# Optimization experiments

Hardware: AMD Instinct MI355X
Metric: run time of the kernel (lower is better)

The kernel has to match this reference:

```python
import jax, jax.numpy as jnp
import numpy as np

NUM_HEADS = 8
NUM_LEVELS = 4
NUM_POINTS = 8
EMBED = 256
SPATIAL_SHAPES = ((92, 160), (46, 80), (23, 40), (12, 20))


def _bilinear_sample(vl, gx, gy, H, W):
    # vl: [N, d, H*W]; gx, gy: [N, Q, P], grid coords in [-1, 1]
    # matches F.grid_sample(mode='bilinear', padding_mode='zeros', align_corners=False)
    x = (gx + 1.0) * (W * 0.5) - 0.5
    y = (gy + 1.0) * (H * 0.5) - 0.5
    x0 = jnp.floor(x)
    y0 = jnp.floor(y)
    wx = x - x0
    wy = y - y0
    x0i = x0.astype(jnp.int32)
    y0i = y0.astype(jnp.int32)
    N, Q, P = gx.shape
    d = vl.shape[1]

    def gather(xi, yi):
        valid = ((xi >= 0) & (xi < W) & (yi >= 0) & (yi < H)).astype(vl.dtype)
        idx = jnp.clip(yi, 0, H - 1) * W + jnp.clip(xi, 0, W - 1)  # [N, Q, P]
        flat = jnp.broadcast_to(idx.reshape(N, 1, Q * P), (N, d, Q * P))
        got = jnp.take_along_axis(vl, flat, axis=2).reshape(N, d, Q, P)
        return got * valid[:, None]

    return (gather(x0i, y0i) * ((1 - wx) * (1 - wy))[:, None]
            + gather(x0i + 1, y0i) * (wx * (1 - wy))[:, None]
            + gather(x0i, y0i + 1) * ((1 - wx) * wy)[:, None]
            + gather(x0i + 1, y0i + 1) * (wx * wy)[:, None])


def _forward(query, value, reference_points, spatial_shapes,
             W_off, b_off, W_attn, b_attn, W_val, b_val, W_out, b_out):
    shapes = np.asarray(spatial_shapes)  # static per-level (H, W)
    bs, Q, C = query.shape
    H, Lv, P = NUM_HEADS, NUM_LEVELS, NUM_POINTS
    d = C // H
    # value projection, split into heads: [bs*H, d, Ltot]
    v = value @ W_val + b_val
    v = v.reshape(bs, -1, H, d).transpose(0, 2, 3, 1).reshape(bs * H, d, -1)
    # sampling offsets [bs, Q, H, Lv, P, 2]
    off = (query @ W_off + b_off).reshape(bs, Q, H, Lv, P, 2)
    # attention weights, softmax over Lv*P
    aw = jax.nn.softmax((query @ W_attn + b_attn).reshape(bs, Q, H, Lv * P), axis=-1)
    aw = aw.reshape(bs, Q, H, Lv, P).transpose(0, 2, 1, 3, 4).reshape(bs * H, Q, Lv, P)
    # normalize offsets by level (W, H)
    norm = jnp.asarray([[w_, h_] for h_, w_ in shapes], dtype=query.dtype)  # [Lv, 2]
    loc = reference_points[:, :, None, :, None, :] + off / norm[None, None, None, :, None, :]
    grids = (2.0 * loc - 1.0).transpose(0, 2, 1, 3, 4, 5).reshape(bs * H, Q, Lv, P, 2)
    out = jnp.zeros((bs * H, d, Q), dtype=query.dtype)
    start = 0
    for lvl in range(Lv):
        H_l, W_l = int(shapes[lvl, 0]), int(shapes[lvl, 1])
        vl = v[:, :, start:start + H_l * W_l]
        g = grids[:, :, lvl]  # [bs*H, Q, P, 2]
        s = _bilinear_sample(vl, g[..., 0], g[..., 1], H_l, W_l)  # [bs*H, d, Q, P]
        out = out + jnp.einsum('ndqp,nqp->ndq', s, aw[:, :, lvl])
        start += H_l * W_l
    out = out.reshape(bs, H, d, Q).transpose(0, 3, 1, 2).reshape(bs, Q, C)
    return out @ W_out + b_out


def setup_inputs() -> dict:
    key = jax.random.key(0)
    ks = jax.random.split(key, 9)
    bs, Q = 6, 4096  # 6 cameras x (64x64 BEV queries)
    Ltot = sum(h * w for h, w in SPATIAL_SHAPES)  # 19560
    HLP2 = NUM_HEADS * NUM_LEVELS * NUM_POINTS * 2  # 512
    HLP = NUM_HEADS * NUM_LEVELS * NUM_POINTS  # 256
    s = 0.02
    return {
        "query": jax.random.normal(ks[0], (bs, Q, EMBED), jnp.float32),
        "value": jax.random.normal(ks[1], (bs, Ltot, EMBED), jnp.float32),
        "reference_points": jax.random.uniform(ks[2], (bs, Q, NUM_LEVELS, 2), jnp.float32),
        "spatial_shapes": jnp.asarray(SPATIAL_SHAPES, jnp.int32),
        "W_off": s * jax.random.normal(ks[3], (EMBED, HLP2), jnp.float32),
        "b_off": s * jax.random.normal(ks[4], (HLP2,), jnp.float32),
        "W_attn": s * jax.random.normal(ks[5], (EMBED, HLP), jnp.float32),
        "b_attn": s * jax.random.normal(ks[6], (HLP,), jnp.float32),
        "W_val": s * jax.random.normal(ks[7], (EMBED, EMBED), jnp.float32),
        "b_val": jnp.zeros((EMBED,), jnp.float32),
        "W_out": s * jax.random.normal(ks[8], (EMBED, EMBED), jnp.float32),
        "b_out": jnp.zeros((EMBED,), jnp.float32),
    }


def reference(query, value, reference_points, spatial_shapes,
              W_off, b_off, W_attn, b_attn, W_val, b_val, W_out, b_out):
    return _forward(query, value, reference_points, spatial_shapes,
                    W_off, b_off, W_attn, b_attn, W_val, b_val, W_out, b_out)
```

## Files before the change

kernel.cpp:

```cpp
#include <hip/hip_runtime.h>
#include <hip/hip_fp16.h>
#include <stdint.h>

#define BS 6
#define NQ 4096
#define NH 8
#define EMB 256
#define LTOT 19560
#define ROWS_V 117360
#define ROWS_VP 117376
#define ROWS_Q 24576
#define VB2 1834
#define QB 1152

typedef __attribute__((ext_vector_type(8))) short bf16x8;
typedef __attribute__((ext_vector_type(4))) float floatx4;
typedef __attribute__((ext_vector_type(8))) unsigned short ushort8v;

__device__ __forceinline__ ushort f2bf(float f) {
    union { float f; uint32_t i; } c; c.f = f;
    uint32_t r = c.i + 0x7FFFu + ((c.i >> 16) & 1u);
    return (ushort)(r >> 16);
}
__device__ __forceinline__ ushort f2h(float f) {
    __half h = __float2half(f);
    union { __half h; ushort u; } c; c.h = h; return c.u;
}
__device__ __forceinline__ float h2f(ushort u) {
    union { ushort u; __half h; } c; c.u = u; return __half2float(c.h);
}
__device__ __forceinline__ uint32_t cvtpk(float a, float b) {
    uint32_t r;
    asm("v_cvt_pk_bf16_f32 %0, %1, %2" : "=v"(r) : "v"(a), "v"(b));
    return r;
}

__device__ __forceinline__ void gll16(const ushort* g, ushort* l) {
    __builtin_amdgcn_global_load_lds(
        (const __attribute__((address_space(1))) void*)g,
        (__attribute__((address_space(3))) void*)l, 16, 0, 0);
}

template<int L>
__device__ __forceinline__ float bcastf(float x) {
    return __int_as_float(
        __builtin_amdgcn_ds_swizzle(__float_as_int(x), 0x1C | (L << 5)));
}
template<int L>
__device__ __forceinline__ uint32_t bcastu(uint32_t x) {
    return (uint32_t)__builtin_amdgcn_ds_swizzle((int)x, 0x1C | (L << 5));
}

__device__ __forceinline__ void fmx_lo(float& acc, float w, uint32_t u) {
    asm("v_fma_mix_f32 %0, %1, %2, %0 op_sel:[0,0,0] op_sel_hi:[0,1,0]"
        : "+v"(acc) : "v"(w), "v"(u));
}
__device__ __forceinline__ void fmx_hi(float& acc, float w, uint32_t u) {
    asm("v_fma_mix_f32 %0, %1, %2, %0 op_sel:[0,1,0] op_sel_hi:[0,1,0]"
        : "+v"(acc) : "v"(w), "v"(u));
}

__global__ __launch_bounds__(256) void prep(
    const float* __restrict__ W_val, const float* __restrict__ W_off,
    const float* __restrict__ W_attn, const float* __restrict__ W_out,
    const float* __restrict__ b_off, const float* __restrict__ b_attn,
    ushort* __restrict__ Wvt, ushort* __restrict__ Wq,
    ushort* __restrict__ Wot, float* __restrict__ bcat)
{
    int id = blockIdx.x * 256 + threadIdx.x;
    if (id < 65536) {
        int n = id >> 8, k = id & 255;
        Wvt[id ^ ((n & 7) << 3)] = f2bf(W_val[k * 256 + n]);
        return;
    }
    id -= 65536;
    if (id < 131072) {
        int n = id >> 8, k = id & 255;
        Wq[id ^ ((n & 7) << 3)] = f2bf(W_off[k * 512 + n]);
        return;
    }
    id -= 131072;
    if (id < 65536) {
        int n = id >> 8, k = id & 255;
        Wq[131072 + (id ^ ((n & 7) << 3))] = f2bf(W_attn[k * 256 + n]);
        return;
    }
    id -= 65536;
    if (id < 65536) {
        int n = id >> 8, k = id & 255;
        Wot[id] = f2bf(W_out[k * 256 + n]);
        return;
    }
    id -= 65536;
    if (id < 768) bcat[id] = (id < 512) ? b_off[id] : b_attn[id - 512];
}

__global__ __launch_bounds__(512, 4) void front(
    const float* __restrict__ value,
    const float* __restrict__ query,
    const ushort* __restrict__ Wvt,
    const ushort* __restrict__ Wq,
    const float* __restrict__ b_val,
    const float* __restrict__ bcat,
    ushort* __restrict__ v_out,
    ushort* __restrict__ qp_out)
{
    __shared__ ushort Bs[128 * 256];

    const int t = threadIdx.x;
    const int w = t >> 6;
    const int lane = t & 63;
    const int bid = blockIdx.x;

    const float* Ap;
    const ushort* Bsrc;
    const float* bias;
    ushort* Cout;
    int Nout, bm, bn, Mrows;
    if (bid < VB2) {
        int m = bid >> 1, nh = bid & 1;
        bm = m * 128; bn = nh * 128;
        Ap = value; Bsrc = Wvt + bn * 256; bias = b_val; Cout = v_out;
        Nout = 256; Mrows = ROWS_V;
    } else {
        int qb = bid - VB2;
        int m = qb / 6, nh = qb - m * 6;
        bm = m * 128; bn = nh * 128;
        Ap = query; Bsrc = Wq + bn * 256; bias = bcat; Cout = qp_out;
        Nout = 768; Mrows = ROWS_Q;
    }

    #pragma unroll
    for (int i = 0; i < 8; ++i)
        gll16(Bsrc + i * 4096 + t * 8, &Bs[i * 4096 + t * 8]);
    __syncthreads();

    const int wm = (w >> 2) * 64;
    const int wn = (w & 3) * 32;
    const int ks = (lane >> 4) * 8;
    const int arow0 = bm + wm + (lane & 15);

    const int nl0 = wn + (lane & 15);
    const int bsw = (nl0 & 7) << 3;
    int bbase[2];
    #pragma unroll
    for (int j = 0; j < 2; ++j)
        bbase[j] = (nl0 + j * 16) * 256 + ks;

    const float* arow_p[4];
    bool rok[4];
    #pragma unroll
    for (int i = 0; i < 4; ++i) {
        int r = arow0 + i * 16;
        rok[i] = r < Mrows;
        arow_p[i] = Ap + (size_t)r * 256 + ks;
    }

    floatx4 acc[4][2] = {};

    for (int kt = 0; kt < 256; kt += 32) {
        bf16x8 a[4], b[2];
        #pragma unroll
        for (int i = 0; i < 4; ++i) {
            float4 f0, f1;
            if (rok[i]) {
                f0 = *(const float4*)(arow_p[i] + kt);
                f1 = *(const float4*)(arow_p[i] + kt + 4);
            } else {
                f0 = make_float4(0.f, 0.f, 0.f, 0.f); f1 = f0;
            }
            union { uint32_t u[4]; bf16x8 v; } cc;
            cc.u[0] = cvtpk(f0.x, f0.y);
            cc.u[1] = cvtpk(f0.z, f0.w);
            cc.u[2] = cvtpk(f1.x, f1.y);
            cc.u[3] = cvtpk(f1.z, f1.w);
            a[i] = cc.v;
        }
        #pragma unroll
        for (int j = 0; j < 2; ++j)
            b[j] = *(const bf16x8*)&Bs[(bbase[j] + kt) ^ bsw];
        #pragma unroll
        for (int i = 0; i < 4; ++i)
            #pragma unroll
            for (int j = 0; j < 2; ++j)
                acc[i][j] = __builtin_amdgcn_mfma_f32_16x16x32_bf16(
                    a[i], b[j], acc[i][j], 0, 0, 0);
    }

    const int crow = (lane >> 4) * 4;
    const int ccol = lane & 15;
    #pragma unroll
    for (int j = 0; j < 2; ++j) {
        int gcol = bn + wn + j * 16 + ccol;
        float bv = bias[gcol];
        #pragma unroll
        for (int i = 0; i < 4; ++i) {
            #pragma unroll
            for (int r = 0; r < 4; ++r) {
                int grow = bm + wm + i * 16 + crow + r;
                if (grow < Mrows)
                    Cout[(size_t)grow * Nout + gcol] = f2h(acc[i][j][r] + bv);
            }
        }
    }
}

__global__ __launch_bounds__(256) void gemm_bt(
    const ushort* __restrict__ A,
    const ushort* __restrict__ Bt,
    const float* __restrict__ bias,
    float* __restrict__ C, int M, int N)
{
    constexpr int K = 256;
    __shared__ ushort As[128 * 32];
    __shared__ ushort Bs[128 * 32];

    const int t = threadIdx.x;
    const int w = t >> 6;
    const int lane = t & 63;
    const int bm = blockIdx.x * 128;
    const int bn = blockIdx.y * 128;
    const int wm = (w >> 1) * 64;
    const int wn = (w & 1) * 64;

    floatx4 acc[4][4] = {};

    const int srow = lane >> 2;
    const int scol = (lane & 3) * 8;
    const ushort* Ag0 = A + (size_t)(bm + (w * 2 + 0) * 16 + srow) * K + scol;
    const ushort* Ag1 = A + (size_t)(bm + (w * 2 + 1) * 16 + srow) * K + scol;
    const ushort* Bg0 = Bt + (size_t)(bn + (w * 2 + 0) * 16 + srow) * K + scol;
    const ushort* Bg1 = Bt + (size_t)(bn + (w * 2 + 1) * 16 + srow) * K + scol;
    ushort* Al0 = &As[(w * 2 + 0) * 512];
    ushort* Al1 = &As[(w * 2 + 1) * 512];
    ushort* Bl0 = &Bs[(w * 2 + 0) * 512];
    ushort* Bl1 = &Bs[(w * 2 + 1) * 512];

    const ushort* apt = &As[(wm + (lane & 15)) * 32 + (lane >> 4) * 8];
    const ushort* bpt = &Bs[(wn + (lane & 15)) * 32 + (lane >> 4) * 8];

    for (int kt = 0; kt < K; kt += 32) {
        __syncthreads();
        gll16(Ag0 + kt, Al0);
        gll16(Ag1 + kt, Al1);
        gll16(Bg0 + kt, Bl0);
        gll16(Bg1 + kt, Bl1);
        __syncthreads();

        bf16x8 a[4], b[4];
        #pragma unroll
        for (int i = 0; i < 4; ++i) {
            a[i] = *(const bf16x8*)(apt + i * 16 * 32);
            b[i] = *(const bf16x8*)(bpt + i * 16 * 32);
        }
        #pragma unroll
        for (int i = 0; i < 4; ++i)
            #pragma unroll
            for (int j = 0; j < 4; ++j)
                acc[i][j] = __builtin_amdgcn_mfma_f32_16x16x32_bf16(
                    a[i], b[j], acc[i][j], 0, 0, 0);
    }

    const int crow = (lane >> 4) * 4;
    const int ccol = lane & 15;
    #pragma unroll
    for (int j = 0; j < 4; ++j) {
        int gcol = bn + wn + j * 16 + ccol;
        float bv = bias[gcol];
        #pragma unroll
        for (int i = 0; i < 4; ++i) {
            #pragma unroll
            for (int r = 0; r < 4; ++r) {
                int grow = bm + wm + i * 16 + crow + r;
                if (grow < M)
                    C[(size_t)grow * N + gcol] = acc[i][j][r] + bv;
            }
        }
    }
}

__global__ __launch_bounds__(256) void sampler4(
    const ushort* __restrict__ v,
    const ushort* __restrict__ qp,
    const float* __restrict__ ref,
    ushort* __restrict__ agg)
{
    __shared__ char ballast[49152];
    if (blockIdx.x > 0x7FFFFFF0u) {
        ballast[threadIdx.x] = (char)threadIdx.x;
        agg[0] = (ushort)ballast[(threadIdx.x * 37) & 4095];
    }

    const int bid = (blockIdx.x & 7) * 384 + (blockIdx.x >> 3);

    const int tid = threadIdx.x;
    const int g = bid * 64 + (tid >> 2);
    const int st = tid & 3;
    const int h = g & 7;
    const int bq = g >> 3;
    const int b = bid >> 9;

    const int Wl = 160 >> st;
    const int Hl = (st == 3) ? 12 : (92 >> st);
    const int Sl = (st == 0) ? 0 : (st == 1) ? 14720 : (st == 2) ? 18400 : 19320;

    const ushort* qrow = qp + (size_t)bq * 768;

    float px[8], py[8];
    {
        ushort8v uo0 = *(const ushort8v*)(qrow + h * 64 + st * 16);
        ushort8v uo1 = *(const ushort8v*)(qrow + h * 64 + st * 16 + 8);
        float2 rf = *(const float2*)(ref + (size_t)bq * 8 + st * 2);
        const float fW = (float)Wl, fH = (float)Hl;
        #pragma unroll
        for (int i = 0; i < 4; ++i) {
            px[i]     = fmaf(rf.x, fW, h2f(uo0[2 * i]))     - 0.5f;
            py[i]     = fmaf(rf.y, fH, h2f(uo0[2 * i + 1])) - 0.5f;
            px[i + 4] = fmaf(rf.x, fW, h2f(uo1[2 * i]))     - 0.5f;
            py[i + 4] = fmaf(rf.y, fH, h2f(uo1[2 * i + 1])) - 0.5f;
        }
    }

    float a8[8];
    {
        ushort8v ul = *(const ushort8v*)(qrow + 512 + h * 32 + st * 8);
        #pragma unroll
        for (int i = 0; i < 8; ++i) a8[i] = h2f(ul[i]);
        float m = a8[0];
        #pragma unroll
        for (int i = 1; i < 8; ++i) m = fmaxf(m, a8[i]);
        m = fmaxf(m, __shfl_xor(m, 1, 4));
        m = fmaxf(m, __shfl_xor(m, 2, 4));
        float s = 0.f;
        #pragma unroll
        for (int i = 0; i < 8; ++i) { a8[i] = __expf(a8[i] - m); s += a8[i]; }
        s += __shfl_xor(s, 1, 4);
        s += __shfl_xor(s, 2, 4);
        float inv = 1.f / s;
        #pragma unroll
        for (int i = 0; i < 8; ++i) a8[i] *= inv;
    }

    const char* vb = (const char*)(v + (size_t)b * (LTOT * EMB));
    const uint32_t coffB = (uint32_t)(h * 64 + st * 16);

    float acc[8] = {0.f, 0.f, 0.f, 0.f, 0.f, 0.f, 0.f, 0.f};

    #pragma unroll
    for (int idx = 0; idx < 8; ++idx) {
        float px_ = px[idx], py_ = py[idx];
        float x0f = floorf(px_), y0f = floorf(py_);
        float wx = px_ - x0f, wy = py_ - y0f;
        int x0 = (int)x0f, y0 = (int)y0f;
        int x1 = x0 + 1, y1 = y0 + 1;
        float vx0 = ((uint32_t)x0 < (uint32_t)Wl) ? 1.f : 0.f;
        float vx1 = ((uint32_t)x1 < (uint32_t)Wl) ? 1.f : 0.f;
        float vy0 = ((uint32_t)y0 < (uint32_t)Hl) ? 1.f : 0.f;
        float vy1 = ((uint32_t)y1 < (uint32_t)Hl) ? 1.f : 0.f;
        int cx0 = min(max(x0, 0), Wl - 1);
        int cx1 = min(max(x1, 0), Wl - 1);
        int cy0 = min(max(y0, 0), Hl - 1);
        int cy1 = min(max(y1, 0), Hl - 1);
        float aw = a8[idx];
        float omx = 1.f - wx, omy = 1.f - wy;
        float omya = omy * aw, wya = wy * aw;
        float w00 = omx * omya * (vx0 * vy0);
        float w10 = wx  * omya * (vx1 * vy0);
        float w01 = omx * wya  * (vx0 * vy1);
        float w11 = wx  * wya  * (vx1 * vy1);
        int r0 = Sl + cy0 * Wl;
        int r1 = Sl + cy1 * Wl;
        uint32_t e00 = (uint32_t)(r0 + cx0) << 9;
        uint32_t e10 = (uint32_t)(r0 + cx1) << 9;
        uint32_t e01 = (uint32_t)(r1 + cx0) << 9;
        uint32_t e11 = (uint32_t)(r1 + cx1) << 9;

        #define ACCMIX(w_, c_) \
            fmx_lo(acc[0], w_, c_.x); fmx_hi(acc[1], w_, c_.x); \
            fmx_lo(acc[2], w_, c_.y); fmx_hi(acc[3], w_, c_.y); \
            fmx_lo(acc[4], w_, c_.z); fmx_hi(acc[5], w_, c_.z); \
            fmx_lo(acc[6], w_, c_.w); fmx_hi(acc[7], w_, c_.w);
        #define DO_LEVEL(L) { \
            float W00 = bcastf<L>(w00), W10 = bcastf<L>(w10); \
            float W01 = bcastf<L>(w01), W11 = bcastf<L>(w11); \
            uint32_t E00 = bcastu<L>(e00), E10 = bcastu<L>(e10); \
            uint32_t E01 = bcastu<L>(e01), E11 = bcastu<L>(e11); \
            uint4 c00 = *(const uint4*)(vb + (E00 + coffB)); \
            uint4 c10 = *(const uint4*)(vb + (E10 + coffB)); \
            uint4 c01 = *(const uint4*)(vb + (E01 + coffB)); \
            uint4 c11 = *(const uint4*)(vb + (E11 + coffB)); \
            ACCMIX(W00, c00); ACCMIX(W10, c10); \
            ACCMIX(W01, c01); ACCMIX(W11, c11); }
        DO_LEVEL(0)
        DO_LEVEL(1)
        DO_LEVEL(2)
        DO_LEVEL(3)
        #undef DO_LEVEL
        #undef ACCMIX
    }

    ushort8v r;
    #pragma unroll
    for (int i = 0; i < 8; ++i) r[i] = f2bf(acc[i]);
    *(ushort8v*)(agg + (size_t)bq * 256 + h * 32 + st * 8) = r;
}

extern "C" void kernel_launch(void* const* d_in, const int* in_sizes, int n_in,
                              void* d_out, int out_size, void* d_ws, size_t ws_size,
                              hipStream_t stream) {
    const float* query  = (const float*)d_in[0];
    const float* value  = (const float*)d_in[1];
    const float* refpts = (const float*)d_in[2];
    const float* W_off  = (const float*)d_in[4];
    const float* b_off  = (const float*)d_in[5];
    const float* W_attn = (const float*)d_in[6];
    const float* b_attn = (const float*)d_in[7];
    const float* W_val  = (const float*)d_in[8];
    const float* b_val  = (const float*)d_in[9];
    const float* W_out  = (const float*)d_in[10];
    const float* b_out  = (const float*)d_in[11];
    float* out = (float*)d_out;

    char* ws = (char*)d_ws;
    ushort* v_bf   = (ushort*)(ws);
    ushort* qp     = (ushort*)(ws + 72679424ull);
    ushort* agg_bf = (ushort*)(ws + 148176896ull);
    ushort* Wvt    = (ushort*)(ws + 160759808ull);
    ushort* Wq     = (ushort*)(ws + 160890880ull);
    ushort* Wot    = (ushort*)(ws + 161284096ull);
    float*  bcat   = (float*) (ws + 161415168ull);

    prep<<<1283, 256, 0, stream>>>(W_val, W_off, W_attn, W_out,
                                   b_off, b_attn, Wvt, Wq, Wot, bcat);

    front<<<VB2 + QB, 512, 0, stream>>>(
        value, query, Wvt, Wq, b_val, bcat, v_bf, qp);

    sampler4<<<(ROWS_Q * NH) / 64, 256, 0, stream>>>(
        v_bf, qp, refpts, agg_bf);

    gemm_bt<<<dim3(ROWS_Q / 128, 2), 256, 0, stream>>>(
        agg_bf, Wot, b_out, out, ROWS_Q, 256);
}
```

Measured before the change: 495.7 us.

## Restructure front GEMM to stage activations in LDS, stream weights from global

The front projection kernel used to stage a 128x256 slice of bf16 weights in LDS and have every wave read and convert fp32 activations straight from global memory. Each block now owns 64 rows covering 256 output columns. The block converts those activation rows to bf16 once into swizzled LDS, in two K halves so the second half's conversion overlaps the first half's MFMAs, and each wave reads its weight fragments directly from global/L2. The aim is to stop redundant global reads and bf16 conversions of activation rows across column tiles, at the cost of more global weight traffic and a 256-thread block with a larger accumulator tile.

```diff
diff --git a/kernel.cpp b/kernel.cpp
--- a/kernel.cpp
+++ b/kernel.cpp
@@ -10,8 +10,8 @@
 #define ROWS_V 117360
 #define ROWS_VP 117376
 #define ROWS_Q 24576
-#define VB2 1834
-#define QB 1152
+#define VB 1834
+#define QB3 1152
 
 typedef __attribute__((ext_vector_type(8))) short bf16x8;
 typedef __attribute__((ext_vector_type(4))) float floatx4;
@@ -70,19 +70,19 @@
     int id = blockIdx.x * 256 + threadIdx.x;
     if (id < 65536) {
         int n = id >> 8, k = id & 255;
-        Wvt[id ^ ((n & 7) << 3)] = f2bf(W_val[k * 256 + n]);
+        Wvt[id] = f2bf(W_val[k * 256 + n]);
         return;
     }
     id -= 65536;
     if (id < 131072) {
         int n = id >> 8, k = id & 255;
-        Wq[id ^ ((n & 7) << 3)] = f2bf(W_off[k * 512 + n]);
+        Wq[id] = f2bf(W_off[k * 512 + n]);
         return;
     }
     id -= 131072;
     if (id < 65536) {
         int n = id >> 8, k = id & 255;
-        Wq[131072 + (id ^ ((n & 7) << 3))] = f2bf(W_attn[k * 256 + n]);
+        Wq[131072 + id] = f2bf(W_attn[k * 256 + n]);
         return;
     }
     id -= 65536;
@@ -95,7 +95,7 @@
     if (id < 768) bcat[id] = (id < 512) ? b_off[id] : b_attn[id - 512];
 }
 
-__global__ __launch_bounds__(512, 4) void front(
+__global__ __launch_bounds__(256, 3) void front(
     const float* __restrict__ value,
     const float* __restrict__ query,
     const ushort* __restrict__ Wvt,
@@ -105,99 +105,135 @@
     ushort* __restrict__ v_out,
     ushort* __restrict__ qp_out)
 {
-    __shared__ ushort Bs[128 * 256];
+    __shared__ ushort As[64 * 256];
 
     const int t = threadIdx.x;
     const int w = t >> 6;
     const int lane = t & 63;
     const int bid = blockIdx.x;
 
-    const float* Ap;
-    const ushort* Bsrc;
-    const float* bias;
-    ushort* Cout;
-    int Nout, bm, bn, Mrows;
-    if (bid < VB2) {
-        int m = bid >> 1, nh = bid & 1;
-        bm = m * 128; bn = nh * 128;
-        Ap = value; Bsrc = Wvt + bn * 256; bias = b_val; Cout = v_out;
+    const float* Ap; const ushort* Bt; const float* bias;
+    ushort* Cout; int Nout, bm, bn, Mrows;
+    if (bid < VB) {
+        bm = bid * 64; bn = 0;
+        Ap = value; Bt = Wvt; bias = b_val; Cout = v_out;
         Nout = 256; Mrows = ROWS_V;
     } else {
-        int qb = bid - VB2;
-        int m = qb / 6, nh = qb - m * 6;
-        bm = m * 128; bn = nh * 128;
-        Ap = query; Bsrc = Wq + bn * 256; bias = bcat; Cout = qp_out;
+        int qb = bid - VB;
+        int m = qb / 3, nh = qb - m * 3;
+        bm = m * 64; bn = nh * 256;
+        Ap = query; Bt = Wq + (size_t)bn * 256; bias = bcat; Cout = qp_out;
         Nout = 768; Mrows = ROWS_Q;
     }
 
-    #pragma unroll
-    for (int i = 0; i < 8; ++i)
-        gll16(Bsrc + i * 4096 + t * 8, &Bs[i * 4096 + t * 8]);
+    const int rt = t >> 2;
+    const int jc = t & 3;
+    const bool rv = (bm + rt) < Mrows;
+    const float* Arow = Ap + (size_t)(bm + rt) * 256;
+    ushort* Aw = As + rt * 256;
+    const int rx = (rt & 7) << 3;
+
+    float4 fa[8], fb[8];
+    #pragma unroll
+    for (int i = 0; i < 4; ++i) {
+        int c = jc + i * 4;
+        if (rv) {
+            fa[2 * i]     = *(const float4*)(Arow + c * 8);
+            fa[2 * i + 1] = *(const float4*)(Arow + c * 8 + 4);
+        } else { fa[2 * i] = make_float4(0.f, 0.f, 0.f, 0.f); fa[2 * i + 1] = fa[2 * i]; }
+    }
+    #pragma unroll
+    for (int i = 0; i < 4; ++i) {
+        int c = 16 + jc + i * 4;
+        if (rv) {
+            fb[2 * i]     = *(const float4*)(Arow + c * 8);
+            fb[2 * i + 1] = *(const float4*)(Arow + c * 8 + 4);
+        } else { fb[2 * i] = make_float4(0.f, 0.f, 0.f, 0.f); fb[2 * i + 1] = fb[2 * i]; }
+    }
+    #pragma unroll
+    for (int i = 0; i < 4; ++i) {
+        int c = jc + i * 4;
+        union { uint32_t u[4]; ushort8v v; } cc;
+        cc.u[0] = cvtpk(fa[2 * i].x,     fa[2 * i].y);
+        cc.u[1] = cvtpk(fa[2 * i].z,     fa[2 * i].w);
+        cc.u[2] = cvtpk(fa[2 * i + 1].x, fa[2 * i + 1].y);
+        cc.u[3] = cvtpk(fa[2 * i + 1].z, fa[2 * i + 1].w);
+        *(ushort8v*)(Aw + ((c * 8) ^ rx)) = cc.v;
+    }
     __syncthreads();
 
-    const int wm = (w >> 2) * 64;
-    const int wn = (w & 3) * 32;
-    const int ks = (lane >> 4) * 8;
-    const int arow0 = bm + wm + (lane & 15);
-
-    const int nl0 = wn + (lane & 15);
-    const int bsw = (nl0 & 7) << 3;
-    int bbase[2];
-    #pragma unroll
-    for (int j = 0; j < 2; ++j)
-        bbase[j] = (nl0 + j * 16) * 256 + ks;
-
-    const float* arow_p[4];
-    bool rok[4];
+    const int wn = w * 64;
+    const ushort* Bw = Bt + (size_t)(wn + (lane & 15)) * 256 + (lane >> 4) * 8;
+    const int ks8 = (lane >> 4) * 8;
+    int arow256[4], rxr[4];
     #pragma unroll
     for (int i = 0; i < 4; ++i) {
-        int r = arow0 + i * 16;
-        rok[i] = r < Mrows;
-        arow_p[i] = Ap + (size_t)r * 256 + ks;
-    }
-
-    floatx4 acc[4][2] = {};
-
-    for (int kt = 0; kt < 256; kt += 32) {
-        bf16x8 a[4], b[2];
-        #pragma unroll
-        for (int i = 0; i < 4; ++i) {
-            float4 f0, f1;
-            if (rok[i]) {
-                f0 = *(const float4*)(arow_p[i] + kt);
-                f1 = *(const float4*)(arow_p[i] + kt + 4);
-            } else {
-                f0 = make_float4(0.f, 0.f, 0.f, 0.f); f1 = f0;
-            }
-            union { uint32_t u[4]; bf16x8 v; } cc;
-            cc.u[0] = cvtpk(f0.x, f0.y);
-            cc.u[1] = cvtpk(f0.z, f0.w);
-            cc.u[2] = cvtpk(f1.x, f1.y);
-            cc.u[3] = cvtpk(f1.z, f1.w);
-            a[i] = cc.v;
-        }
-        #pragma unroll
-        for (int j = 0; j < 2; ++j)
-            b[j] = *(const bf16x8*)&Bs[(bbase[j] + kt) ^ bsw];
+        int row = i * 16 + (lane & 15);
+        arow256[i] = row * 256;
+        rxr[i] = (row & 7) << 3;
+    }
+
+    floatx4 acc[4][4] = {};
+
+    #pragma unroll
+    for (int s = 0; s < 4; ++s) {
+        int kt = s * 32;
+        bf16x8 a[4], b[4];
+        #pragma unroll
+        for (int i = 0; i < 4; ++i)
+            a[i] = *(const bf16x8*)&As[arow256[i] + (((kt + ks8)) ^ rxr[i])];
+        #pragma unroll
+        for (int j = 0; j < 4; ++j)
+            b[j] = *(const bf16x8*)(Bw + (size_t)(j * 16) * 256 + kt);
         #pragma unroll
         for (int i = 0; i < 4; ++i)
             #pragma unroll
-            for (int j = 0; j < 2; ++j)
+            for (int j = 0; j < 4; ++j)
                 acc[i][j] = __builtin_amdgcn_mfma_f32_16x16x32_bf16(
                     a[i], b[j], acc[i][j], 0, 0, 0);
     }
 
+    #pragma unroll
+    for (int i = 0; i < 4; ++i) {
+        int c = 16 + jc + i * 4;
+        union { uint32_t u[4]; ushort8v v; } cc;
+        cc.u[0] = cvtpk(fb[2 * i].x,     fb[2 * i].y);
+        cc.u[1] = cvtpk(fb[2 * i].z,     fb[2 * i].w);
+        cc.u[2] = cvtpk(fb[2 * i + 1].x, fb[2 * i + 1].y);
+        cc.u[3] = cvtpk(fb[2 * i + 1].z, fb[2 * i + 1].w);
+        *(ushort8v*)(Aw + ((c * 8) ^ rx)) = cc.v;
+    }
+    __syncthreads();
+
+    #pragma unroll
+    for (int s = 0; s < 4; ++s) {
+        int kt = 128 + s * 32;
+        bf16x8 a[4], b[4];
+        #pragma unroll
+        for (int i = 0; i < 4; ++i)
+            a[i] = *(const bf16x8*)&As[arow256[i] + (((kt + ks8)) ^ rxr[i])];
+        #pragma unroll
+        for (int j = 0; j < 4; ++j)
+            b[j] = *(const bf16x8*)(Bw + (size_t)(j * 16) * 256 + kt);
+        #pragma unroll
+        for (int i = 0; i < 4; ++i)
+            #pragma unroll
+            for (int j = 0; j < 4; ++j)
+                acc[i][j] = __builtin_amdgcn_mfma_f32_16x16x32_bf16(
+                    a[i], b[j], acc[i][j], 0, 0, 0);
+    }
+
     const int crow = (lane >> 4) * 4;
     const int ccol = lane & 15;
     #pragma unroll
-    for (int j = 0; j < 2; ++j) {
+    for (int j = 0; j < 4; ++j) {
         int gcol = bn + wn + j * 16 + ccol;
         float bv = bias[gcol];
         #pragma unroll
         for (int i = 0; i < 4; ++i) {
             #pragma unroll
             for (int r = 0; r < 4; ++r) {
-                int grow = bm + wm + i * 16 + crow + r;
+                int grow = bm + i * 16 + crow + r;
                 if (grow < Mrows)
                     Cout[(size_t)grow * Nout + gcol] = f2h(acc[i][j][r] + bv);
             }
@@ -433,7 +469,7 @@
     prep<<<1283, 256, 0, stream>>>(W_val, W_off, W_attn, W_out,
                                    b_off, b_attn, Wvt, Wq, Wot, bcat);
 
-    front<<<VB2 + QB, 512, 0, stream>>>(
+    front<<<VB + QB3, 256, 0, stream>>>(
         value, query, Wvt, Wq, b_val, bcat, v_bf, qp);
 
     sampler4<<<(ROWS_Q * NH) / 64, 256, 0, stream>>>(
```

Measured after the change: 424.0 us. 1.17x faster.
